# Optimization experiments

Hardware: AMD Instinct MI355X
Metric: run time of the kernel (lower is better)

The kernel has to match this reference:

```python
import jax, jax.numpy as jnp
import numpy as np

N_NODES = 50000
N_EDGES = 800000
F_DIM = 128
H_DIM = 128


def setup_inputs() -> dict:
    key = jax.random.key(0)
    ks = jax.random.split(key, 14)
    sx = 1.0 / np.sqrt(F_DIM)
    sh = 1.0 / np.sqrt(H_DIM)
    return {
        'x': jax.random.normal(ks[0], (N_NODES, F_DIM), jnp.float32),
        'edge_index': jax.random.randint(ks[1], (2, N_EDGES), 0, N_NODES),
        'edge_weight': jnp.zeros((N_EDGES,), jnp.int32),  # relation ids, all 0 (num_relations=1)
        'h': jax.random.normal(ks[2], (N_NODES, H_DIM), jnp.float32),
        'c': jax.random.normal(ks[3], (N_NODES, H_DIM), jnp.float32),
        # stacked gate params, gate order: i, f, c, o
        'Wx': jax.random.normal(ks[4], (4, F_DIM, H_DIM), jnp.float32) * sx,
        'Wx_root': jax.random.normal(ks[5], (4, F_DIM, H_DIM), jnp.float32) * sx,
        'bx': jax.random.normal(ks[6], (4, H_DIM), jnp.float32) * 0.01,
        'Wh': jax.random.normal(ks[7], (4, H_DIM, H_DIM), jnp.float32) * sh,
        'Wh_root': jax.random.normal(ks[8], (4, H_DIM, H_DIM), jnp.float32) * sh,
        'bh': jax.random.normal(ks[9], (4, H_DIM), jnp.float32) * 0.01,
        'fc_w': jax.random.normal(ks[10], (1, H_DIM), jnp.float32) * sh,
        'fc_b': jax.random.normal(ks[11], (1,), jnp.float32) * 0.01,
    }


def _mean_agg(v, src, dst, n_nodes):
    # scatter-mean of gathered source features onto destination nodes
    s = jax.ops.segment_sum(v[src], dst, num_segments=n_nodes)          # [N, d]
    cnt = jax.ops.segment_sum(jnp.ones(src.shape, v.dtype), dst, num_segments=n_nodes)
    return s / jnp.maximum(cnt, 1.0)[:, None]


def reference(x, edge_index, edge_weight, h, c, Wx, Wx_root, bx, Wh, Wh_root, bh, fc_w, fc_b):
    src, dst = edge_index[0], edge_index[1]
    # single-relation RGCNConv: mean-agg then matmul; aggregation shared across the 4 gates
    agg_x = _mean_agg(x, src, dst, N_NODES)   # [N, F]
    agg_h = _mean_agg(h, src, dst, N_NODES)   # [N, H]
    g = (jnp.einsum('nf,gfh->gnh', agg_x, Wx)
         + jnp.einsum('nf,gfh->gnh', x, Wx_root) + bx[:, None, :]
         + jnp.einsum('nk,gkh->gnh', agg_h, Wh)
         + jnp.einsum('nk,gkh->gnh', h, Wh_root) + bh[:, None, :])  # [4, N, H]
    i_g = jax.nn.sigmoid(g[0])
    f_g = jax.nn.sigmoid(g[1])
    t_g = jnp.tanh(g[2])
    o_g = jax.nn.sigmoid(g[3])
    c_new = f_g * c + i_g * t_g
    h_new = o_g * jnp.tanh(c_new)
    y = jax.nn.relu(h_new) @ fc_w.T + fc_b    # [N, 1]
    return (y, h_new, c_new)
```

## Files before the change

kernel.cpp:

```cpp
#include <hip/hip_runtime.h>
#include <hip/hip_bf16.h>

#define N_NODES 50000
#define N_EDGES 800000
#define FD 128
#define HD 128
#define KTOT 512
#define NTOT 512
#define NRT 391
#define RT_PER_XCD 49
#define SCAN_BLK 1024
#define NSCAN ((N_NODES + SCAN_BLK - 1) / SCAN_BLK)

typedef __attribute__((ext_vector_type(8))) short short8v;
typedef __attribute__((ext_vector_type(8))) __bf16 bf16x8;
typedef __attribute__((ext_vector_type(4))) float f32x4;
typedef __attribute__((ext_vector_type(4))) int i32x4;

__device__ __forceinline__ short f2bf(float f) {
  unsigned u = __builtin_bit_cast(unsigned, f);
  unsigned r = (u + 0x7FFFu + ((u >> 16) & 1u)) >> 16;
  return (short)(r & 0xFFFFu);
}
__device__ __forceinline__ float bf2f(short s) {
  return __builtin_bit_cast(float, ((unsigned)(unsigned short)s) << 16);
}
__device__ __forceinline__ float sigm(float x) {
  return __builtin_amdgcn_rcpf(1.f + __builtin_amdgcn_exp2f(-1.44269504f * x));
}
__device__ __forceinline__ float tanh_(float x) {
  return 1.f - 2.f * __builtin_amdgcn_rcpf(1.f + __builtin_amdgcn_exp2f(2.88539009f * x));
}

__device__ __forceinline__ int swz_col(int c, int r7) {
  return (c & ~63) | (((((c >> 3) & 7) ^ r7)) << 3) | (c & 7);
}

__device__ __forceinline__ void gload_lds16(const void* g, void* l) {
  __builtin_amdgcn_global_load_lds((const __attribute__((address_space(1))) unsigned int*)g,
                                   (__attribute__((address_space(3))) unsigned int*)l, 16, 0, 0);
}

__global__ void k_pre(const float* __restrict__ Wx, const float* __restrict__ Wxr,
                      const float* __restrict__ Wh, const float* __restrict__ Whr,
                      const float* __restrict__ x, const float* __restrict__ h,
                      short* __restrict__ BpackT, short* __restrict__ Apack) {
  int gid = blockIdx.x * 256 + threadIdx.x;
  if (gid < NTOT * KTOT) {
    int col = gid >> 9;
    int k = gid & 511;
    int hb = col >> 7, rem = col & 127;
    int g = rem >> 5, hlow = rem & 31;
    int hid = hb * 32 + hlow;
    int sel = k >> 7, f = k & 127;
    const float* W = (sel == 0) ? Wx : (sel == 1) ? Wxr : (sel == 2) ? Wh : Whr;
    BpackT[col * KTOT + swz_col(k, col & 7)] = f2bf(W[(g * 128 + f) * 128 + hid]);
  }
  if (gid < N_NODES * 32) {
    int half = gid >= N_NODES * 16;
    int g2 = gid - half * N_NODES * 16;
    int node = g2 >> 4, s = g2 & 15;
    const float* src = (half ? h : x) + (size_t)node * 128 + s * 8;
    f32x4 v0 = *(const f32x4*)(src);
    f32x4 v1 = *(const f32x4*)(src + 4);
    short8v o;
#pragma unroll
    for (int q = 0; q < 4; ++q) { o[q] = f2bf(v0[q]); o[q + 4] = f2bf(v1[q]); }
    int blockbase = 128 + half * 256 + (s >> 3) * 64;
    int slot = (s & 7) ^ (node & 7);
    *(short8v*)(Apack + (size_t)node * KTOT + blockbase + slot * 8) = o;
  }
}

__global__ void k_count(const int* __restrict__ ei, int* __restrict__ cnt,
                        int* __restrict__ rank) {
  int e = blockIdx.x * 256 + threadIdx.x;
  if (e < N_EDGES) rank[e] = atomicAdd(&cnt[ei[N_EDGES + e]], 1);
}

__global__ void k_scanA(const int* __restrict__ cnt, int* __restrict__ bsum) {
  int blk = blockIdx.x, t = threadIdx.x;
  int base = blk * SCAN_BLK + t * 4;
  int s = 0;
  if (base + 3 < N_NODES) {
    i32x4 v = *(const i32x4*)(cnt + base);
    s = v.x + v.y + v.z + v.w;
  }
#pragma unroll
  for (int d = 1; d < 64; d <<= 1) s += __shfl_xor(s, d);
  __shared__ int ws[4];
  if ((t & 63) == 0) ws[t >> 6] = s;
  __syncthreads();
  if (t == 0) bsum[blk] = ws[0] + ws[1] + ws[2] + ws[3];
}

__global__ void k_scanC(const int* __restrict__ cnt, const int* __restrict__ bsum,
                        int* __restrict__ off) {
  __shared__ int sboff[NSCAN];
  int blk = blockIdx.x, t = threadIdx.x;
  if (t < 64) {
    int v = (t < NSCAN) ? bsum[t] : 0;
#pragma unroll
    for (int d = 1; d < 64; d <<= 1) {
      int u = __shfl_up(v, d);
      if (t >= d) v += u;
    }
    if (t < NSCAN) sboff[t] = v;
  }
  __syncthreads();
  int base = blk * SCAN_BLK + t * 4;
  int c0 = 0, c1 = 0, c2 = 0, c3 = 0;
  bool ok = base + 3 < N_NODES;
  if (ok) {
    i32x4 v = *(const i32x4*)(cnt + base);
    c0 = v.x; c1 = v.y; c2 = v.z; c3 = v.w;
  }
  int s = c0 + c1 + c2 + c3;
  int v = s;
#pragma unroll
  for (int d = 1; d < 64; d <<= 1) {
    int u = __shfl_up(v, d);
    if ((t & 63) >= d) v += u;
  }
  __shared__ int wsum[4];
  if ((t & 63) == 63) wsum[t >> 6] = v;
  __syncthreads();
  int wbase = 0;
  for (int w = 0; w < (t >> 6); ++w) wbase += wsum[w];
  int excl = (blk ? sboff[blk - 1] : 0) + wbase + v - s;
  if (ok) {
    i32x4 o = {excl, excl + c0, excl + c0 + c1, excl + c0 + c1 + c2};
    *(i32x4*)(off + base) = o;
  }
  if (blk == 0 && t == 0) off[N_NODES] = N_EDGES;
}

__global__ void k_fill(const int* __restrict__ ei, const int* __restrict__ off,
                       const int* __restrict__ rank, int* __restrict__ elist) {
  int e = blockIdx.x * 256 + threadIdx.x;
  if (e < N_EDGES) {
    int d = ei[N_EDGES + e];
    elist[off[d] + rank[e]] = ei[e];
  }
}

__global__ __launch_bounds__(256) void k_agg_pack(const int* __restrict__ off,
                                                  const int* __restrict__ elist,
                                                  short* __restrict__ Apack) {
  int tid = threadIdx.x;
  int node = blockIdx.x * 4 + (tid >> 6);
  int lane = tid & 63;
  int grp = lane >> 4, l4 = lane & 15;
  int is_h = grp & 1, epair = grp >> 1;
  int b = off[node], e = off[node + 1];
  const int cb = is_h * 256 + 128 + (l4 >> 3) * 64;
  const int sl = l4 & 7;
  float acc[8] = {};
  int j = b;
  for (; j + 8 <= e; j += 8) {
    int s0 = elist[j + epair];
    int s1 = elist[j + 2 + epair];
    int s2 = elist[j + 4 + epair];
    int s3 = elist[j + 6 + epair];
    short8v v0 = *(const short8v*)(Apack + (size_t)s0 * KTOT + cb + ((sl ^ (s0 & 7)) << 3));
    short8v v1 = *(const short8v*)(Apack + (size_t)s1 * KTOT + cb + ((sl ^ (s1 & 7)) << 3));
    short8v v2 = *(const short8v*)(Apack + (size_t)s2 * KTOT + cb + ((sl ^ (s2 & 7)) << 3));
    short8v v3 = *(const short8v*)(Apack + (size_t)s3 * KTOT + cb + ((sl ^ (s3 & 7)) << 3));
#pragma unroll
    for (int q = 0; q < 8; ++q) acc[q] += bf2f(v0[q]);
#pragma unroll
    for (int q = 0; q < 8; ++q) acc[q] += bf2f(v1[q]);
#pragma unroll
    for (int q = 0; q < 8; ++q) acc[q] += bf2f(v2[q]);
#pragma unroll
    for (int q = 0; q < 8; ++q) acc[q] += bf2f(v3[q]);
  }
  for (; j + 2 <= e; j += 2) {
    int s0 = elist[j + epair];
    short8v v0 = *(const short8v*)(Apack + (size_t)s0 * KTOT + cb + ((sl ^ (s0 & 7)) << 3));
#pragma unroll
    for (int q = 0; q < 8; ++q) acc[q] += bf2f(v0[q]);
  }
  if (j < e && epair == 0) {
    int s0 = elist[j];
    short8v v0 = *(const short8v*)(Apack + (size_t)s0 * KTOT + cb + ((sl ^ (s0 & 7)) << 3));
#pragma unroll
    for (int q = 0; q < 8; ++q) acc[q] += bf2f(v0[q]);
  }
#pragma unroll
  for (int q = 0; q < 8; ++q) acc[q] += __shfl_xor(acc[q], 32);
  if (grp < 2) {
    float inv = 1.f / (float)max(e - b, 1);
    int cagg = is_h * 256 + (l4 >> 3) * 64 + ((sl ^ (node & 7)) << 3);
    short8v o;
#pragma unroll
    for (int q = 0; q < 8; ++q) o[q] = f2bf(acc[q] * inv);
    *(short8v*)(Apack + (size_t)node * KTOT + cagg) = o;
  }
}

__global__ __launch_bounds__(512, 4) void k_gemm(
    const short* __restrict__ Apack, const short* __restrict__ BpackT,
    const float* __restrict__ c_in, const float* __restrict__ bx, const float* __restrict__ bh,
    const float* __restrict__ fcw,
    float* __restrict__ hnew, float* __restrict__ cnew, float* __restrict__ ypart) {
  __shared__ short As[2][128 * 64];
  __shared__ short Bs[2][128 * 64];
  const int bid = blockIdx.x;
  const int xcd = bid & 7, q = bid >> 3;
  const int rt = xcd * RT_PER_XCD + (q >> 2);
  const int hb = q & 3;
  if (rt >= NRT) return;
  const int tid = threadIdx.x;
  const int wave = tid >> 6, lane = tid & 63;
  const int l15 = lane & 15, lhi = lane >> 4;
  const int row0 = rt * 128;

  const short* Abase = Apack + (size_t)row0 * KTOT;
  const short* Bbase = BpackT + (size_t)hb * 128 * KTOT;
  const int stg_r = tid >> 3;
  const int stg_s = tid & 7;
  const int ldst = (tid & ~63) * 8;

  auto stage = [&](int buf, int k0) {
#pragma unroll
    for (int it = 0; it < 2; ++it) {
      int r = stg_r + it * 64;
      gload_lds16(Abase + (size_t)r * KTOT + k0 + stg_s * 8, &As[buf][ldst + it * 4096]);
      gload_lds16(Bbase + (size_t)r * KTOT + k0 + stg_s * 8, &Bs[buf][ldst + it * 4096]);
    }
  };

  const int rbase = row0 + wave * 16 + lhi * 4;
  const int hid0 = hb * 32 + l15;
  float pbi[2], pbf[2], pbt[2], pbo[2], pfw[2];
#pragma unroll
  for (int n1 = 0; n1 < 2; ++n1) {
    int hid = hid0 + n1 * 16;
    pbi[n1] = bx[hid] + bh[hid];
    pbf[n1] = bx[128 + hid] + bh[128 + hid];
    pbt[n1] = bx[256 + hid] + bh[256 + hid];
    pbo[n1] = bx[384 + hid] + bh[384 + hid];
    pfw[n1] = fcw[hid];
  }
  float cpre[2][4];
#pragma unroll
  for (int n1 = 0; n1 < 2; ++n1)
#pragma unroll
    for (int j = 0; j < 4; ++j) {
      int r = rbase + j;
      cpre[n1][j] = (r < N_NODES) ? c_in[(size_t)r * HD + hid0 + n1 * 16] : 0.f;
    }

  f32x4 acc[8] = {};

  stage(0, 0);
  __syncthreads();
  int cur = 0;
#pragma unroll
  for (int k0 = 0; k0 < KTOT; k0 += 64) {
    if (k0 + 64 < KTOT) stage(cur ^ 1, k0 + 64);
#pragma unroll
    for (int kk = 0; kk < 2; ++kk) {
      short8v a, bfr[8];
      const int sl = ((kk << 2) | lhi) ^ (l15 & 7);
      a = *(const short8v*)(&As[cur][(wave * 16 + l15) * 64 + sl * 8]);
#pragma unroll
      for (int n = 0; n < 8; ++n) {
        int rb = n * 16 + l15;
        bfr[n] = *(const short8v*)(&Bs[cur][rb * 64 + sl * 8]);
      }
#pragma unroll
      for (int n = 0; n < 8; ++n)
        acc[n] = __builtin_amdgcn_mfma_f32_16x16x32_bf16(
            __builtin_bit_cast(bf16x8, a), __builtin_bit_cast(bf16x8, bfr[n]),
            acc[n], 0, 0, 0);
    }
    __syncthreads();
    cur ^= 1;
  }

  float yp[4] = {};
#pragma unroll
  for (int n1 = 0; n1 < 2; ++n1) {
    int hid = hid0 + n1 * 16;
    f32x4 gi = acc[0 + n1], gf = acc[2 + n1], gt = acc[4 + n1], go = acc[6 + n1];
#pragma unroll
    for (int j = 0; j < 4; ++j) {
      int r = rbase + j;
      bool ok = r < N_NODES;
      float cv = cpre[n1][j];
      float ig = sigm(gi[j] + pbi[n1]);
      float fg = sigm(gf[j] + pbf[n1]);
      float tg = tanh_(gt[j] + pbt[n1]);
      float og = sigm(go[j] + pbo[n1]);
      float cn = fg * cv + ig * tg;
      float hn = og * tanh_(cn);
      if (ok) {
        cnew[(size_t)r * HD + hid] = cn;
        hnew[(size_t)r * HD + hid] = hn;
      }
      yp[j] += fmaxf(hn, 0.f) * pfw[n1];
    }
  }
#pragma unroll
  for (int j = 0; j < 4; ++j) {
    float v = yp[j];
    v += __shfl_xor(v, 1);
    v += __shfl_xor(v, 2);
    v += __shfl_xor(v, 4);
    v += __shfl_xor(v, 8);
    if (l15 == 0) {
      int r = rbase + j;
      if (r < N_NODES) ypart[hb * N_NODES + r] = v;
    }
  }
}

__global__ void k_yfinal(const float* __restrict__ ypart, const float* __restrict__ fcb,
                         float* __restrict__ y) {
  int i = blockIdx.x * 256 + threadIdx.x;
  if (i < N_NODES)
    y[i] = fcb[0] + ypart[i] + ypart[N_NODES + i] + ypart[2 * N_NODES + i] + ypart[3 * N_NODES + i];
}

extern "C" void kernel_launch(void* const* d_in, const int* in_sizes, int n_in,
                              void* d_out, int out_size, void* d_ws, size_t ws_size,
                              hipStream_t stream) {
  const float* x   = (const float*)d_in[0];
  const int*   ei  = (const int*)d_in[1];
  const float* h   = (const float*)d_in[3];
  const float* c   = (const float*)d_in[4];
  const float* Wx  = (const float*)d_in[5];
  const float* Wxr = (const float*)d_in[6];
  const float* bx  = (const float*)d_in[7];
  const float* Wh  = (const float*)d_in[8];
  const float* Whr = (const float*)d_in[9];
  const float* bh  = (const float*)d_in[10];
  const float* fcw = (const float*)d_in[11];
  const float* fcb = (const float*)d_in[12];

  float* y    = (float*)d_out;
  float* hnew = y + N_NODES;
  float* cnew = hnew + (size_t)N_NODES * HD;

  char* w = (char*)d_ws;
  auto carve = [&](size_t bytes) {
    char* p = w;
    w += (bytes + 255) & ~(size_t)255;
    return p;
  };
  int* cnt      = (int*)carve((size_t)N_NODES * 4);
  int* off      = (int*)carve((size_t)(N_NODES + 1) * 4);
  int* pos      = (int*)carve((size_t)N_NODES * 4);
  int* elist    = (int*)carve((size_t)N_EDGES * 4);
  short* Apack  = (short*)carve((size_t)N_NODES * KTOT * 2);
  short* BpackT = (short*)carve((size_t)NTOT * KTOT * 2);
  float* ypart  = (float*)carve((size_t)4 * N_NODES * 4);
  int* bsum     = (int*)ypart;
  int* rank     = (int*)Apack;
  (void)pos;

  hipMemsetAsync(cnt, 0, (size_t)N_NODES * 4, stream);
  k_count<<<(N_EDGES + 255) / 256, 256, 0, stream>>>(ei, cnt, rank);
  k_scanA<<<NSCAN, 256, 0, stream>>>(cnt, bsum);
  k_scanC<<<NSCAN, 256, 0, stream>>>(cnt, bsum, off);
  k_fill<<<(N_EDGES + 255) / 256, 256, 0, stream>>>(ei, off, rank, elist);
  k_pre<<<(N_NODES * 32 + 255) / 256, 256, 0, stream>>>(Wx, Wxr, Wh, Whr, x, h, BpackT, Apack);
  k_agg_pack<<<(N_NODES + 3) / 4, 256, 0, stream>>>(off, elist, Apack);
  dim3 gg(8 * RT_PER_XCD * 4);
  k_gemm<<<gg, 512, 0, stream>>>(Apack, BpackT, c, bx, bh, fcw, hnew, cnew, ypart);
  k_yfinal<<<(N_NODES + 255) / 256, 256, 0, stream>>>(ypart, fcb, y);
}
```

Before: 180.0 us.

## Retile GEMM waves as 4x2 grid to cut LDS B-fragment reads

Changes the per-wave tile from 16 rows x 128 columns to 32 rows x 64 columns, with 4 waves along M and 2 along N. The packed B layout is re-permuted so each wave's 64 columns hold all four gates for 16 hidden units. Per k-step each wave now does 6 LDS fragment reads instead of 9 for the same 8 MFMAs, which lowers LDS bandwidth pressure. The fc partial sum now needs a cross-wave reduction through shared memory plus an extra barrier.

New measurement: 179.0 us. No clear change (-0.6%).

```diff
diff --git a/kernel.cpp b/kernel.cpp
--- a/kernel.cpp
+++ b/kernel.cpp
@@ -50,8 +50,8 @@
     int col = gid >> 9;
     int k = gid & 511;
     int hb = col >> 7, rem = col & 127;
-    int g = rem >> 5, hlow = rem & 31;
-    int hid = hb * 32 + hlow;
+    int wn = rem >> 6, g = (rem >> 4) & 3, hlow = rem & 15;
+    int hid = hb * 32 + wn * 16 + hlow;
     int sel = k >> 7, f = k & 127;
     const float* W = (sel == 0) ? Wx : (sel == 1) ? Wxr : (sel == 2) ? Wh : Whr;
     BpackT[col * KTOT + swz_col(k, col & 7)] = f2bf(W[(g * 128 + f) * 128 + hid]);
@@ -214,6 +214,7 @@
   const int tid = threadIdx.x;
   const int wave = tid >> 6, lane = tid & 63;
   const int l15 = lane & 15, lhi = lane >> 4;
+  const int wm = wave & 3, wn = wave >> 2;
   const int row0 = rt * 128;
 
   const short* Abase = Apack + (size_t)row0 * KTOT;
@@ -231,28 +232,23 @@
     }
   };
 
-  const int rbase = row0 + wave * 16 + lhi * 4;
-  const int hid0 = hb * 32 + l15;
-  float pbi[2], pbf[2], pbt[2], pbo[2], pfw[2];
-#pragma unroll
-  for (int n1 = 0; n1 < 2; ++n1) {
-    int hid = hid0 + n1 * 16;
-    pbi[n1] = bx[hid] + bh[hid];
-    pbf[n1] = bx[128 + hid] + bh[128 + hid];
-    pbt[n1] = bx[256 + hid] + bh[256 + hid];
-    pbo[n1] = bx[384 + hid] + bh[384 + hid];
-    pfw[n1] = fcw[hid];
-  }
+  const int rbase = row0 + wm * 32 + lhi * 4;
+  const int hid = hb * 32 + wn * 16 + l15;
+  float pbi = bx[hid] + bh[hid];
+  float pbf = bx[128 + hid] + bh[128 + hid];
+  float pbt = bx[256 + hid] + bh[256 + hid];
+  float pbo = bx[384 + hid] + bh[384 + hid];
+  float pfw = fcw[hid];
   float cpre[2][4];
 #pragma unroll
-  for (int n1 = 0; n1 < 2; ++n1)
+  for (int m = 0; m < 2; ++m)
 #pragma unroll
     for (int j = 0; j < 4; ++j) {
-      int r = rbase + j;
-      cpre[n1][j] = (r < N_NODES) ? c_in[(size_t)r * HD + hid0 + n1 * 16] : 0.f;
-    }
-
-  f32x4 acc[8] = {};
+      int r = rbase + m * 16 + j;
+      cpre[m][j] = (r < N_NODES) ? c_in[(size_t)r * HD + hid] : 0.f;
+    }
+
+  f32x4 acc[2][4] = {};
 
   stage(0, 0);
   __syncthreads();
@@ -262,58 +258,75 @@
     if (k0 + 64 < KTOT) stage(cur ^ 1, k0 + 64);
 #pragma unroll
     for (int kk = 0; kk < 2; ++kk) {
-      short8v a, bfr[8];
+      short8v a[2], bfr[4];
       const int sl = ((kk << 2) | lhi) ^ (l15 & 7);
-      a = *(const short8v*)(&As[cur][(wave * 16 + l15) * 64 + sl * 8]);
-#pragma unroll
-      for (int n = 0; n < 8; ++n) {
-        int rb = n * 16 + l15;
-        bfr[n] = *(const short8v*)(&Bs[cur][rb * 64 + sl * 8]);
-      }
-#pragma unroll
-      for (int n = 0; n < 8; ++n)
-        acc[n] = __builtin_amdgcn_mfma_f32_16x16x32_bf16(
-            __builtin_bit_cast(bf16x8, a), __builtin_bit_cast(bf16x8, bfr[n]),
-            acc[n], 0, 0, 0);
+#pragma unroll
+      for (int m = 0; m < 2; ++m)
+        a[m] = *(const short8v*)(&As[cur][(wm * 32 + m * 16 + l15) * 64 + sl * 8]);
+#pragma unroll
+      for (int n = 0; n < 4; ++n)
+        bfr[n] = *(const short8v*)(&Bs[cur][(wn * 64 + n * 16 + l15) * 64 + sl * 8]);
+#pragma unroll
+      for (int m = 0; m < 2; ++m)
+#pragma unroll
+        for (int n = 0; n < 4; ++n)
+          acc[m][n] = __builtin_amdgcn_mfma_f32_16x16x32_bf16(
+              __builtin_bit_cast(bf16x8, a[m]), __builtin_bit_cast(bf16x8, bfr[n]),
+              acc[m][n], 0, 0, 0);
     }
     __syncthreads();
     cur ^= 1;
   }
 
-  float yp[4] = {};
-#pragma unroll
-  for (int n1 = 0; n1 < 2; ++n1) {
-    int hid = hid0 + n1 * 16;
-    f32x4 gi = acc[0 + n1], gf = acc[2 + n1], gt = acc[4 + n1], go = acc[6 + n1];
+  float yp[2][4];
+#pragma unroll
+  for (int m = 0; m < 2; ++m) {
 #pragma unroll
     for (int j = 0; j < 4; ++j) {
-      int r = rbase + j;
+      int r = rbase + m * 16 + j;
       bool ok = r < N_NODES;
-      float cv = cpre[n1][j];
-      float ig = sigm(gi[j] + pbi[n1]);
-      float fg = sigm(gf[j] + pbf[n1]);
-      float tg = tanh_(gt[j] + pbt[n1]);
-      float og = sigm(go[j] + pbo[n1]);
-      float cn = fg * cv + ig * tg;
+      float ig = sigm(acc[m][0][j] + pbi);
+      float fg = sigm(acc[m][1][j] + pbf);
+      float tg = tanh_(acc[m][2][j] + pbt);
+      float og = sigm(acc[m][3][j] + pbo);
+      float cn = fg * cpre[m][j] + ig * tg;
       float hn = og * tanh_(cn);
       if (ok) {
         cnew[(size_t)r * HD + hid] = cn;
         hnew[(size_t)r * HD + hid] = hn;
       }
-      yp[j] += fmaxf(hn, 0.f) * pfw[n1];
-    }
-  }
-#pragma unroll
-  for (int j = 0; j < 4; ++j) {
-    float v = yp[j];
-    v += __shfl_xor(v, 1);
-    v += __shfl_xor(v, 2);
-    v += __shfl_xor(v, 4);
-    v += __shfl_xor(v, 8);
-    if (l15 == 0) {
-      int r = rbase + j;
-      if (r < N_NODES) ypart[hb * N_NODES + r] = v;
-    }
+      yp[m][j] = fmaxf(hn, 0.f) * pfw;
+    }
+  }
+#pragma unroll
+  for (int m = 0; m < 2; ++m)
+#pragma unroll
+    for (int j = 0; j < 4; ++j) {
+      float v = yp[m][j];
+      v += __shfl_xor(v, 1);
+      v += __shfl_xor(v, 2);
+      v += __shfl_xor(v, 4);
+      v += __shfl_xor(v, 8);
+      yp[m][j] = v;
+    }
+  float* yred = (float*)&As[0][0];
+  if (wn == 1 && l15 == 0) {
+#pragma unroll
+    for (int m = 0; m < 2; ++m)
+#pragma unroll
+      for (int j = 0; j < 4; ++j)
+        yred[wm * 32 + m * 16 + lhi * 4 + j] = yp[m][j];
+  }
+  __syncthreads();
+  if (wn == 0 && l15 == 0) {
+#pragma unroll
+    for (int m = 0; m < 2; ++m)
+#pragma unroll
+      for (int j = 0; j < 4; ++j) {
+        int r = rbase + m * 16 + j;
+        if (r < N_NODES)
+          ypart[hb * N_NODES + r] = yp[m][j] + yred[wm * 32 + m * 16 + lhi * 4 + j];
+      }
   }
 }
 
```
